# Kernel tuning notes

Hardware: AMD Instinct MI355X
Metric: run time of the kernel (lower is better)

## Reference

```python
import jax, jax.numpy as jnp
import numpy as np

B, C, H, W = 2048, 4, 84, 84
FEAT = 7 * 7 * 64  # 3136, from 84->20->9->7 conv arithmetic
D = 512
E = 6            # num_experts
K = 2            # top_k
A = 12           # output_dim (actions)


def _conv(x, w, b, stride):
    y = jax.lax.conv_general_dilated(
        x, w, window_strides=(stride, stride), padding='VALID',
        dimension_numbers=('NCHW', 'OIHW', 'NCHW'))
    return y + b[None, :, None, None]


def setup_inputs() -> dict:
    key = jax.random.key(0)
    ks = jax.random.split(key, 16)
    s = lambda k, shape, fan: jax.random.normal(k, shape, jnp.float32) * (1.0 / np.sqrt(fan))
    return {
        'x': jax.random.normal(ks[0], (B, C, H, W), jnp.float32),
        'c1_w': s(ks[1], (32, C, 8, 8), C * 64), 'c1_b': jnp.zeros((32,), jnp.float32),
        'c2_w': s(ks[2], (64, 32, 4, 4), 32 * 16), 'c2_b': jnp.zeros((64,), jnp.float32),
        'c3_w': s(ks[3], (64, 64, 3, 3), 64 * 9), 'c3_b': jnp.zeros((64,), jnp.float32),
        'fc_w': s(ks[4], (FEAT, D), FEAT), 'fc_b': jnp.zeros((D,), jnp.float32),
        'gate_w': s(ks[5], (D, E), D), 'gate_b': jnp.zeros((E,), jnp.float32),
        'e_w1': s(ks[6], (E, D, D), D), 'e_b1': jnp.zeros((E, D), jnp.float32),
        'e_w2': s(ks[7], (E, D, D), D), 'e_b2': jnp.zeros((E, D), jnp.float32),
        'e_w3': s(ks[8], (E, D, A), D), 'e_b3': jnp.zeros((E, A), jnp.float32),
    }


def reference(x, c1_w, c1_b, c2_w, c2_b, c3_w, c3_b, fc_w, fc_b,
              gate_w, gate_b, e_w1, e_b1, e_w2, e_b2, e_w3, e_b3):
    # CNN feature extractor (dropout omitted: eval semantics)
    h = jax.nn.relu(_conv(x, c1_w, c1_b, 4))
    h = jax.nn.relu(_conv(h, c2_w, c2_b, 2))
    h = jax.nn.relu(_conv(h, c3_w, c3_b, 1))
    h = h.reshape(h.shape[0], -1)                     # [B, 3136] (C,H,W flatten order)
    f = jax.nn.relu(h @ fc_w + fc_b)                  # [B, 512]

    # Gating: softmax -> top-2 -> renormalize
    gate_probs = jax.nn.softmax(f @ gate_w + gate_b, axis=-1)    # [B, E]
    top_p, top_i = jax.lax.top_k(gate_probs, K)                   # [B, K]
    top_p = top_p / jnp.sum(top_p, axis=-1, keepdims=True)

    # Experts: compute all (tiny MLPs), then gather top-k outputs
    h1 = jax.nn.relu(jnp.einsum('bd,edh->beh', f, e_w1) + e_b1)   # [B, E, D]
    h2 = jax.nn.relu(jnp.einsum('beh,ehg->beg', h1, e_w2) + e_b2) # [B, E, D]
    eo = jnp.einsum('beg,ego->beo', h2, e_w3) + e_b3              # [B, E, A]
    sel = jnp.take_along_axis(eo, top_i[:, :, None], axis=1)      # [B, K, A]
    out = jnp.sum(sel * top_p[:, :, None], axis=1)                # [B, A]
    return out
```

## Files before the change

### kernel.cpp

```cpp
#include <hip/hip_runtime.h>
#include <hip/hip_bf16.h>
#include <math.h>

typedef __attribute__((ext_vector_type(8))) short bf16x8;
typedef __attribute__((ext_vector_type(4))) float f32x4;

__device__ __forceinline__ float b2f(unsigned short u) {
    unsigned int v = ((unsigned int)u) << 16;
    return __uint_as_float(v);
}
__device__ __forceinline__ unsigned short f2b(float f) {
    __hip_bfloat16 h = __float2bfloat16(f);
    return *reinterpret_cast<unsigned short*>(&h);
}
__device__ __forceinline__ void split_trunc(float v, short& h, short& l) {
    unsigned int ui = __float_as_uint(v);
    h = (short)(ui >> 16);
    float hf = __uint_as_float(ui & 0xffff0000u);
    l = (short)f2b(v - hf);
}

__global__ __launch_bounds__(256) void prep_w(
    const float* __restrict__ w1, const float* __restrict__ w2, const float* __restrict__ w3,
    const float* __restrict__ ew3,
    unsigned short* __restrict__ wb1h, unsigned short* __restrict__ wb1l,
    unsigned short* __restrict__ w2h, unsigned short* __restrict__ w2l,
    unsigned short* __restrict__ w3h, unsigned short* __restrict__ w3l,
    float* __restrict__ w3t) {
    int tid = blockIdx.x * 256 + threadIdx.x;
    if (tid < 8192) {
        int k = tid >> 8, r = tid & 255;
        int c = r >> 6, ky = (r >> 3) & 7, kx = r & 7;
        float v = w1[tid];
        unsigned short h = f2b(v);
        int d = ((ky * 2 + (k >> 4)) * 16 + (k & 15)) * 32 + c * 8 + kx;
        wb1h[d] = h;
        wb1l[d] = f2b(v - b2f(h));
    } else if (tid < 8192 + 32768) {
        int i = tid - 8192;
        int n = i >> 9, r = i & 511;
        int c = r >> 4, ky = (r >> 2) & 3, kx = r & 3;
        float v = w2[i];
        unsigned short h = f2b(v);
        int d = ((ky * 4 + kx) * 64 + n) * 32 + c;
        w2h[d] = h;
        w2l[d] = f2b(v - b2f(h));
    } else if (tid < 8192 + 32768 + 36864) {
        int i = tid - 40960;
        int n = i / 576, r = i - n * 576;
        int c = r / 9, s = r - c * 9;
        int ky = s / 3, kx = s - ky * 3;
        float v = w3[i];
        unsigned short h = f2b(v);
        int d = (((ky * 3 + kx) * 2 + (c >> 5)) * 64 + n) * 32 + (c & 31);
        w3h[d] = h;
        w3l[d] = f2b(v - b2f(h));
    } else if (tid < 77824 + 36864) {
        int i = tid - 77824;
        int e = i / 6144, rem = i - e * 6144;
        int a = rem >> 9, k = rem & 511;
        w3t[i] = ew3[e * 6144 + k * 12 + a];
    }
}

__global__ __launch_bounds__(256) void prep_fcw(
    const float* __restrict__ fw, unsigned short* __restrict__ h, unsigned short* __restrict__ l) {
    __shared__ float tile[64][65];
    int k0 = blockIdx.x * 64;
    int n0 = blockIdx.y * 64;
    int tx = threadIdx.x & 63, ty = threadIdx.x >> 6;
#pragma unroll
    for (int j = 0; j < 16; j++) {
        int kk = ty + j * 4;
        int kp = k0 + kk;
        int p = kp >> 6, c = kp & 63;
        tile[kk][tx] = fw[(c * 49 + p) * 512 + n0 + tx];
    }
    __syncthreads();
#pragma unroll
    for (int j = 0; j < 16; j++) {
        int r = ty + j * 4;
        float v = tile[tx][r];
        unsigned short hh = f2b(v);
        long d = (long)(n0 + r) * 3136 + k0 + tx;
        h[d] = hh;
        l[d] = f2b(v - b2f(hh));
    }
}

__global__ __launch_bounds__(256) void prep_ewT(
    const float* __restrict__ ew1, const float* __restrict__ ew2,
    unsigned short* __restrict__ t1, unsigned short* __restrict__ t2) {
    __shared__ float tile[32][33];
    int z = blockIdx.z;
    int e = z % 6;
    const float* src = (z < 6) ? (ew1 + e * 262144) : (ew2 + e * 262144);
    unsigned short* dst = (z < 6) ? (t1 + e * 262144) : (t2 + e * 262144);
    int d0 = blockIdx.y * 32;
    int h0 = blockIdx.x * 32;
    int tx = threadIdx.x, ty = threadIdx.y;
#pragma unroll
    for (int j = 0; j < 4; j++)
        tile[ty + j * 8][tx] = src[(d0 + ty + j * 8) * 512 + h0 + tx];
    __syncthreads();
#pragma unroll
    for (int j = 0; j < 4; j++)
        dst[(h0 + ty + j * 8) * 512 + (d0 + tx)] = f2b(tile[tx][ty + j * 8]);
}

__global__ __launch_bounds__(256, 4) void conv1_k(
    const float* __restrict__ x, const unsigned short* __restrict__ wbh,
    const unsigned short* __restrict__ wbl, const float* __restrict__ b1,
    unsigned short* __restrict__ yhi, unsigned short* __restrict__ ylo) {
    __shared__ bf16x8 wlds[8][4][64];
    int t = threadIdx.x;
    {
        int tab = t >> 6, ln = t & 63;
        const unsigned short* sb = ((tab < 2) ? wbh : wbl) +
            ((ln & 15) * 32 + (ln >> 4) * 8 + (tab & 1) * 512);
#pragma unroll
        for (int k = 0; k < 8; k++)
            wlds[k][tab][ln] = *(const bf16x8*)(sb + k * 1024);
    }
    int wave = t >> 6, lane = t & 63, l16 = lane & 15, quad = lane >> 4;
    int px0 = blockIdx.x * 128 + wave * 32;
    const float* abase[2];
#pragma unroll
    for (int i = 0; i < 2; i++) {
        int px = px0 + i * 16 + l16;
        int n = px / 400;
        int rem = px - n * 400;
        int oy = rem / 20;
        int ox = rem - oy * 20;
        abase[i] = x + (long)n * 28224 + quad * 7056 + oy * 4 * 84 + ox * 4;
    }
    f32x4 acc[2][2];
#pragma unroll
    for (int i = 0; i < 2; i++)
#pragma unroll
        for (int j = 0; j < 2; j++)
#pragma unroll
            for (int r = 0; r < 4; r++) acc[i][j][r] = 0.f;
    __syncthreads();
    float4 buf[3][4];
#pragma unroll
    for (int r = 0; r < 2; r++) {
        __builtin_amdgcn_sched_barrier(0);
#pragma unroll
        for (int i = 0; i < 2; i++) {
            const float* p = abase[i] + r * 84;
            buf[r][i * 2] = *(const float4*)p;
            buf[r][i * 2 + 1] = *(const float4*)(p + 4);
        }
        __builtin_amdgcn_sched_barrier(0);
    }
#pragma unroll
    for (int ky = 0; ky < 8; ky++) {
        if (ky < 6) {
            __builtin_amdgcn_sched_barrier(0);
#pragma unroll
            for (int i = 0; i < 2; i++) {
                const float* p = abase[i] + (ky + 2) * 84;
                buf[(ky + 2) % 3][i * 2] = *(const float4*)p;
                buf[(ky + 2) % 3][i * 2 + 1] = *(const float4*)(p + 4);
            }
            __builtin_amdgcn_sched_barrier(0);
        }
        bf16x8 bh0 = wlds[ky][0][lane];
        bf16x8 bh1 = wlds[ky][1][lane];
        bf16x8 bl0 = wlds[ky][2][lane];
        bf16x8 bl1 = wlds[ky][3][lane];
        bf16x8 ah[2], al[2];
#pragma unroll
        for (int i = 0; i < 2; i++) {
            const float4& c0 = buf[ky % 3][i * 2];
            const float4& c1 = buf[ky % 3][i * 2 + 1];
            float v[8] = {c0.x, c0.y, c0.z, c0.w, c1.x, c1.y, c1.z, c1.w};
#pragma unroll
            for (int j = 0; j < 8; j++) {
                short hh, ll;
                split_trunc(v[j], hh, ll);
                ah[i][j] = hh;
                al[i][j] = ll;
            }
        }
#pragma unroll
        for (int i = 0; i < 2; i++) {
            acc[i][0] = __builtin_amdgcn_mfma_f32_16x16x32_bf16(ah[i], bh0, acc[i][0], 0, 0, 0);
            acc[i][0] = __builtin_amdgcn_mfma_f32_16x16x32_bf16(al[i], bh0, acc[i][0], 0, 0, 0);
            acc[i][0] = __builtin_amdgcn_mfma_f32_16x16x32_bf16(ah[i], bl0, acc[i][0], 0, 0, 0);
            acc[i][1] = __builtin_amdgcn_mfma_f32_16x16x32_bf16(ah[i], bh1, acc[i][1], 0, 0, 0);
            acc[i][1] = __builtin_amdgcn_mfma_f32_16x16x32_bf16(al[i], bh1, acc[i][1], 0, 0, 0);
            acc[i][1] = __builtin_amdgcn_mfma_f32_16x16x32_bf16(ah[i], bl1, acc[i][1], 0, 0, 0);
        }
    }
    float bias0 = b1[l16], bias1 = b1[16 + l16];
#pragma unroll
    for (int i = 0; i < 2; i++) {
#pragma unroll
        for (int r = 0; r < 4; r++) {
            long px = px0 + i * 16 + quad * 4 + r;
            long o = px * 32;
            float v0 = fmaxf(acc[i][0][r] + bias0, 0.f);
            float v1 = fmaxf(acc[i][1][r] + bias1, 0.f);
            short h0, l0, h1, l1;
            split_trunc(v0, h0, l0);
            split_trunc(v1, h1, l1);
            yhi[o + l16] = (unsigned short)h0;
            ylo[o + l16] = (unsigned short)l0;
            yhi[o + 16 + l16] = (unsigned short)h1;
            ylo[o + 16 + l16] = (unsigned short)l1;
        }
    }
}

template <int C, int IH, int IW, int OH, int OW, int S, int KH, int KW>
__global__ __launch_bounds__(256, 2) void convm_k(
    const unsigned short* __restrict__ xhi, const unsigned short* __restrict__ xlo,
    const unsigned short* __restrict__ whi, const unsigned short* __restrict__ wlo,
    const float* __restrict__ bias,
    unsigned short* __restrict__ yhi, unsigned short* __restrict__ ylo) {
    constexpr int CH = C / 32;
    constexpr int NCHUNK = KH * KW * CH;
    __shared__ unsigned short Bst[2][2][4][64][8];
    int t = threadIdx.x;
    int wave = t >> 6, lane = t & 63, l16 = lane & 15, quad = lane >> 4;
    int pxbase = blockIdx.x * 256 + wave * 64;
    long xoff[4];
#pragma unroll
    for (int i = 0; i < 4; i++) {
        int px = pxbase + i * 16 + l16;
        int n = px / (OH * OW);
        int rem = px - n * (OH * OW);
        int oy = rem / OW;
        int ox = rem - oy * OW;
        xoff[i] = (((long)n * IH + oy * S) * IW + ox * S) * C + quad * 8;
    }
    f32x4 acc[4][4];
#pragma unroll
    for (int i = 0; i < 4; i++)
#pragma unroll
        for (int j = 0; j < 4; j++)
#pragma unroll
            for (int r = 0; r < 4; r++) acc[i][j][r] = 0.f;
    long wsrc = (long)lane * 32 + wave * 8;
    uint4 sh = *(const uint4*)(whi + wsrc);
    uint4 sl = *(const uint4*)(wlo + wsrc);
    bf16x8 a_h[4], a_l[4];
    {
#pragma unroll
        for (int i = 0; i < 4; i++) {
            a_h[i] = *(const bf16x8*)(xhi + xoff[i]);
            a_l[i] = *(const bf16x8*)(xlo + xoff[i]);
        }
    }
    *(uint4*)&Bst[0][0][wave][lane][0] = sh;
    *(uint4*)&Bst[0][1][wave][lane][0] = sl;
    asm volatile("s_waitcnt lgkmcnt(0)\n\ts_barrier" ::: "memory");
#pragma unroll
    for (int ck = 0; ck < NCHUNK; ck++) {
        const int cur = ck & 1;
        uint4 nsh, nsl;
        bf16x8 na_h[4], na_l[4];
        if (ck + 1 < NCHUNK) {
            long ws = (long)(ck + 1) * 2048 + lane * 32 + wave * 8;
            nsh = *(const uint4*)(whi + ws);
            nsl = *(const uint4*)(wlo + ws);
            int ck1 = ck + 1;
            int kyx = ck1 / CH;
            int ch = ck1 - kyx * CH;
            int ky = kyx / KW, kx = kyx - ky * KW;
            long k1 = ((long)(ky * IW + kx)) * C + ch * 32;
#pragma unroll
            for (int i = 0; i < 4; i++) {
                na_h[i] = *(const bf16x8*)(xhi + xoff[i] + k1);
                na_l[i] = *(const bf16x8*)(xlo + xoff[i] + k1);
            }
        }
        bf16x8 bh[4], bl[4];
#pragma unroll
        for (int j = 0; j < 4; j++) {
            bh[j] = *(const bf16x8*)&Bst[cur][0][quad][j * 16 + l16][0];
            bl[j] = *(const bf16x8*)&Bst[cur][1][quad][j * 16 + l16][0];
        }
#pragma unroll
        for (int i = 0; i < 4; i++)
#pragma unroll
            for (int j = 0; j < 4; j++) {
                acc[i][j] = __builtin_amdgcn_mfma_f32_16x16x32_bf16(a_h[i], bh[j], acc[i][j], 0, 0, 0);
                acc[i][j] = __builtin_amdgcn_mfma_f32_16x16x32_bf16(a_h[i], bl[j], acc[i][j], 0, 0, 0);
                acc[i][j] = __builtin_amdgcn_mfma_f32_16x16x32_bf16(a_l[i], bh[j], acc[i][j], 0, 0, 0);
            }
        if (ck + 1 < NCHUNK) {
            __builtin_amdgcn_sched_barrier(0);
            *(uint4*)&Bst[cur ^ 1][0][wave][lane][0] = nsh;
            *(uint4*)&Bst[cur ^ 1][1][wave][lane][0] = nsl;
            asm volatile("s_waitcnt lgkmcnt(0)\n\ts_barrier" ::: "memory");
#pragma unroll
            for (int i = 0; i < 4; i++) {
                a_h[i] = na_h[i];
                a_l[i] = na_l[i];
            }
        }
    }
#pragma unroll
    for (int i = 0; i < 4; i++)
#pragma unroll
        for (int j = 0; j < 4; j++) {
            int col = j * 16 + l16;
            float bv = bias[col];
#pragma unroll
            for (int r = 0; r < 4; r++) {
                int prow = pxbase + i * 16 + quad * 4 + r;
                float v = fmaxf(acc[i][j][r] + bv, 0.f);
                unsigned short h = f2b(v);
                yhi[(long)prow * 64 + col] = h;
                ylo[(long)prow * 64 + col] = f2b(v - b2f(h));
            }
        }
}

__global__ __launch_bounds__(64, 3) void fc_k(
    const unsigned short* __restrict__ Ahi, const unsigned short* __restrict__ Alo,
    const unsigned short* __restrict__ Bhi, const unsigned short* __restrict__ Blo,
    float* __restrict__ Cp) {
    int lane = threadIdx.x, l16 = lane & 15, quad = lane >> 4;
    int m0 = blockIdx.x * 64, n0 = blockIdx.y * 64;
    int z = blockIdx.z;
    int kBase = z * 448;
    f32x4 acc[4][4];
#pragma unroll
    for (int i = 0; i < 4; i++)
#pragma unroll
        for (int j = 0; j < 4; j++)
#pragma unroll
            for (int r = 0; r < 4; r++) acc[i][j][r] = 0.f;
#pragma unroll 2
    for (int k0 = kBase; k0 < kBase + 448; k0 += 32) {
        bf16x8 ah[4], al[4], bh[4], bl[4];
#pragma unroll
        for (int i = 0; i < 4; i++) {
            long a = (long)(m0 + i * 16 + l16) * 3136 + k0 + quad * 8;
            ah[i] = *(const bf16x8*)(Ahi + a);
            al[i] = *(const bf16x8*)(Alo + a);
        }
#pragma unroll
        for (int j = 0; j < 4; j++) {
            long b = (long)(n0 + j * 16 + l16) * 3136 + k0 + quad * 8;
            bh[j] = *(const bf16x8*)(Bhi + b);
            bl[j] = *(const bf16x8*)(Blo + b);
        }
#pragma unroll
        for (int i = 0; i < 4; i++)
#pragma unroll
            for (int j = 0; j < 4; j++) {
                acc[i][j] = __builtin_amdgcn_mfma_f32_16x16x32_bf16(ah[i], bh[j], acc[i][j], 0, 0, 0);
                acc[i][j] = __builtin_amdgcn_mfma_f32_16x16x32_bf16(ah[i], bl[j], acc[i][j], 0, 0, 0);
                acc[i][j] = __builtin_amdgcn_mfma_f32_16x16x32_bf16(al[i], bh[j], acc[i][j], 0, 0, 0);
            }
    }
    float* Cz = Cp + (long)z * 1048576;
#pragma unroll
    for (int i = 0; i < 4; i++)
#pragma unroll
        for (int j = 0; j < 4; j++) {
            int col = n0 + j * 16 + l16;
#pragma unroll
            for (int r = 0; r < 4; r++) {
                int row = m0 + i * 16 + quad * 4 + r;
                Cz[row * 512 + col] = acc[i][j][r];
            }
        }
}

__global__ __launch_bounds__(256) void fc_fin(
    const float* __restrict__ Cp, const float* __restrict__ bias,
    float* __restrict__ f, unsigned short* __restrict__ fb, int* __restrict__ cnt) {
    if (blockIdx.x == 0 && threadIdx.x < 8) cnt[threadIdx.x] = 0;
    int tid = blockIdx.x * 256 + threadIdx.x;
    int col = tid & 511;
    float v = bias[col];
#pragma unroll
    for (int z = 0; z < 7; z++) v += Cp[tid + (long)z * 1048576];
    v = fmaxf(v, 0.f);
    f[tid] = v;
    fb[tid] = f2b(v);
}

__global__ __launch_bounds__(256) void gate_k(
    const float* __restrict__ f, const float* __restrict__ gw, const float* __restrict__ gb,
    int* __restrict__ topi, float* __restrict__ topp,
    int* __restrict__ cnt, int* __restrict__ rowlist, int* __restrict__ slotp) {
    int wave = threadIdx.x >> 6, lane = threadIdx.x & 63;
    int row = blockIdx.x * 4 + wave;
    float fv[8];
#pragma unroll
    for (int j = 0; j < 8; j++) fv[j] = f[row * 512 + lane + 64 * j];
    float lg[6];
#pragma unroll
    for (int e = 0; e < 6; e++) {
        float a = 0.f;
#pragma unroll
        for (int j = 0; j < 8; j++) a += fv[j] * gw[(lane + 64 * j) * 6 + e];
#pragma unroll
        for (int off = 32; off > 0; off >>= 1) a += __shfl_xor(a, off, 64);
        lg[e] = a + gb[e];
    }
    if (lane == 0) {
        int i1 = 0;
        float v1 = lg[0];
#pragma unroll
        for (int e = 1; e < 6; e++)
            if (lg[e] > v1) { v1 = lg[e]; i1 = e; }
        int i2 = (i1 == 0) ? 1 : 0;
        float v2 = lg[i2];
#pragma unroll
        for (int e = 0; e < 6; e++)
            if (e != i1 && lg[e] > v2) { v2 = lg[e]; i2 = e; }
        float pa = 1.f / (1.f + expf(v2 - v1));
        topi[row * 2] = i1;
        topi[row * 2 + 1] = i2;
        topp[row * 2] = pa;
        topp[row * 2 + 1] = 1.f - pa;
        int s1 = atomicAdd(cnt + i1, 1);
        int s2 = atomicAdd(cnt + i2, 1);
        rowlist[i1 * 2048 + s1] = row;
        rowlist[i2 * 2048 + s2] = row;
        slotp[row * 2] = s1;
        slotp[row * 2 + 1] = s2;
    }
}

__global__ __launch_bounds__(64, 4) void moe_gemm(
    const unsigned short* __restrict__ A, long aStride,
    const unsigned short* __restrict__ Bt, const float* __restrict__ bias,
    unsigned short* __restrict__ C,
    const int* __restrict__ cnt, const int* __restrict__ rowlist) {
    int e = blockIdx.z;
    int ne = cnt[e];
    int m0 = blockIdx.x * 64;
    if (m0 >= ne) return;
    const unsigned short* Ae = A + (long)e * aStride;
    const unsigned short* Be = Bt + (long)e * 262144;
    const float* be = bias + e * 512;
    unsigned short* Ce = C + (long)e * 2048 * 512;
    int lane = threadIdx.x, l16 = lane & 15, quad = lane >> 4;
    int n0 = blockIdx.y * 64;
    int arow[4];
#pragma unroll
    for (int i = 0; i < 4; i++) {
        int slot = m0 + i * 16 + l16;
        arow[i] = rowlist ? ((slot < ne) ? rowlist[e * 2048 + slot] : 0) : slot;
    }
    f32x4 acc[4][4];
#pragma unroll
    for (int i = 0; i < 4; i++)
#pragma unroll
        for (int j = 0; j < 4; j++)
#pragma unroll
            for (int r = 0; r < 4; r++) acc[i][j][r] = 0.f;
#pragma unroll 4
    for (int k0 = 0; k0 < 512; k0 += 32) {
        bf16x8 a[4], b[4];
#pragma unroll
        for (int i = 0; i < 4; i++)
            a[i] = *(const bf16x8*)(Ae + (long)arow[i] * 512 + k0 + quad * 8);
#pragma unroll
        for (int j = 0; j < 4; j++)
            b[j] = *(const bf16x8*)(Be + (long)(n0 + j * 16 + l16) * 512 + k0 + quad * 8);
#pragma unroll
        for (int i = 0; i < 4; i++)
#pragma unroll
            for (int j = 0; j < 4; j++)
                acc[i][j] = __builtin_amdgcn_mfma_f32_16x16x32_bf16(a[i], b[j], acc[i][j], 0, 0, 0);
    }
#pragma unroll
    for (int i = 0; i < 4; i++)
#pragma unroll
        for (int j = 0; j < 4; j++) {
            int col = n0 + j * 16 + l16;
            float bcol = be[col];
#pragma unroll
            for (int r = 0; r < 4; r++) {
                int row = m0 + i * 16 + quad * 4 + r;
                float v = fmaxf(acc[i][j][r] + bcol, 0.f);
                Ce[(long)row * 512 + col] = f2b(v);
            }
        }
}

__global__ __launch_bounds__(256) void combine_k(
    const unsigned short* __restrict__ h2, const float* __restrict__ w3t,
    const float* __restrict__ b3, const int* __restrict__ topi,
    const float* __restrict__ topp, const int* __restrict__ slotp,
    float* __restrict__ out) {
    int b = blockIdx.x * 4 + (threadIdx.x >> 6);
    int lane = threadIdx.x & 63;
    int e0 = topi[b * 2], e1 = topi[b * 2 + 1];
    float p0 = topp[b * 2], p1 = topp[b * 2 + 1];
    int s0 = slotp[b * 2], s1 = slotp[b * 2 + 1];
    float r[12];
#pragma unroll
    for (int a = 0; a < 12; a++) r[a] = 0.f;
#pragma unroll
    for (int j = 0; j < 2; j++) {
        int e = j ? e1 : e0;
        int s = j ? s1 : s0;
        float p = j ? p1 : p0;
        const unsigned short* hp = h2 + ((long)e * 2048 + s) * 512 + lane * 8;
        bf16x8 hv = *(const bf16x8*)hp;
        float hf[8];
#pragma unroll
        for (int q = 0; q < 8; q++) hf[q] = b2f((unsigned short)hv[q]);
        const float* wb = w3t + e * 6144 + lane * 8;
#pragma unroll
        for (int a = 0; a < 12; a++) {
            float4 w0 = *(const float4*)(wb + a * 512);
            float4 w1 = *(const float4*)(wb + a * 512 + 4);
            float acc = hf[0] * w0.x + hf[1] * w0.y + hf[2] * w0.z + hf[3] * w0.w +
                        hf[4] * w1.x + hf[5] * w1.y + hf[6] * w1.z + hf[7] * w1.w;
            r[a] += p * acc;
        }
    }
#pragma unroll
    for (int a = 0; a < 12; a++)
#pragma unroll
        for (int off = 32; off > 0; off >>= 1) r[a] += __shfl_xor(r[a], off, 64);
    float v = 0.f;
#pragma unroll
    for (int a = 0; a < 12; a++)
        if (lane == a) v = r[a];
    if (lane < 12)
        out[b * 12 + lane] = v + p0 * b3[e0 * 12 + lane] + p1 * b3[e1 * 12 + lane];
}

extern "C" void kernel_launch(void* const* d_in, const int* in_sizes, int n_in,
                              void* d_out, int out_size, void* d_ws, size_t ws_size,
                              hipStream_t stream) {
    const float* x   = (const float*)d_in[0];
    const float* c1w = (const float*)d_in[1];
    const float* c1b = (const float*)d_in[2];
    const float* c2w = (const float*)d_in[3];
    const float* c2b = (const float*)d_in[4];
    const float* c3w = (const float*)d_in[5];
    const float* c3b = (const float*)d_in[6];
    const float* fcw = (const float*)d_in[7];
    const float* fcb = (const float*)d_in[8];
    const float* gw  = (const float*)d_in[9];
    const float* gb  = (const float*)d_in[10];
    const float* ew1 = (const float*)d_in[11];
    const float* eb1 = (const float*)d_in[12];
    const float* ew2 = (const float*)d_in[13];
    const float* eb2 = (const float*)d_in[14];
    const float* ew3 = (const float*)d_in[15];
    const float* eb3 = (const float*)d_in[16];

    char* ws = (char*)d_ws;
    unsigned short* y1hi = (unsigned short*)(ws + 0L);
    unsigned short* y1lo = (unsigned short*)(ws + 52428800L);
    unsigned short* f3hi = (unsigned short*)(ws + 0L);
    unsigned short* f3lo = (unsigned short*)(ws + 12845056L);
    int*   cnt           = (int*)(ws + 26214400L);
    int*   rowlist       = (int*)(ws + 26214464L);
    int*   slotp         = (int*)(ws + 26263616L);
    unsigned short* y2hi = (unsigned short*)(ws + 104857600L);
    unsigned short* y2lo = (unsigned short*)(ws + 126091264L);
    unsigned short* h1   = (unsigned short*)(ws + 104857600L);
    unsigned short* h2   = (unsigned short*)(ws + 117440512L);
    float* f             = (float*)(ws + 147324928L);
    unsigned short* fb   = (unsigned short*)(ws + 151519232L);
    int*   topi          = (int*)(ws + 153616384L);
    float* topp          = (float*)(ws + 153632768L);
    unsigned short* w2h  = (unsigned short*)(ws + 153681920L);
    unsigned short* w2l  = (unsigned short*)(ws + 153747456L);
    unsigned short* w3h  = (unsigned short*)(ws + 153812992L);
    unsigned short* w3l  = (unsigned short*)(ws + 153886720L);
    unsigned short* fcwh = (unsigned short*)(ws + 153960448L);
    unsigned short* fcwl = (unsigned short*)(ws + 157171712L);
    unsigned short* ew1t = (unsigned short*)(ws + 160382976L);
    unsigned short* ew2t = (unsigned short*)(ws + 163528704L);
    float* w3t           = (float*)(ws + 166674432L);
    float* Cp            = (float*)(ws + 166821888L);
    unsigned short* wb1h = (unsigned short*)(ws + 196182016L);
    unsigned short* wb1l = (unsigned short*)(ws + 196198400L);
    float* out = (float*)d_out;

    hipLaunchKernelGGL(prep_w, dim3(448), dim3(256), 0, stream, c1w, c2w, c3w, ew3,
                       wb1h, wb1l, w2h, w2l, w3h, w3l, w3t);
    hipLaunchKernelGGL(prep_fcw, dim3(49, 8), dim3(256), 0, stream, fcw, fcwh, fcwl);
    hipLaunchKernelGGL(prep_ewT, dim3(16, 16, 12), dim3(32, 8), 0, stream, ew1, ew2, ew1t, ew2t);
    hipLaunchKernelGGL(conv1_k, dim3(6400), dim3(256), 0, stream, x, wb1h, wb1l, c1b, y1hi, y1lo);
    hipLaunchKernelGGL((convm_k<32, 20, 20, 9, 9, 2, 4, 4>), dim3(648), dim3(256), 0, stream,
                       y1hi, y1lo, w2h, w2l, c2b, y2hi, y2lo);
    hipLaunchKernelGGL((convm_k<64, 9, 9, 7, 7, 1, 3, 3>), dim3(392), dim3(256), 0, stream,
                       y2hi, y2lo, w3h, w3l, c3b, f3hi, f3lo);
    hipLaunchKernelGGL(fc_k, dim3(32, 8, 7), dim3(64), 0, stream, f3hi, f3lo, fcwh, fcwl, Cp);
    hipLaunchKernelGGL(fc_fin, dim3(4096), dim3(256), 0, stream, Cp, fcb, f, fb, cnt);
    hipLaunchKernelGGL(gate_k, dim3(512), dim3(256), 0, stream, f, gw, gb, topi, topp,
                       cnt, rowlist, slotp);
    hipLaunchKernelGGL(moe_gemm, dim3(32, 8, 6), dim3(64), 0, stream, fb, 0L, ew1t, eb1, h1,
                       cnt, rowlist);
    hipLaunchKernelGGL(moe_gemm, dim3(32, 8, 6), dim3(64), 0, stream, h1, 1048576L, ew2t, eb2, h2,
                       cnt, (const int*)nullptr);
    hipLaunchKernelGGL(combine_k, dim3(512), dim3(256), 0, stream, h2, w3t, eb3, topi, topp,
                       slotp, out);
}
```

Before: 693.8 us.

## Merge prep kernels, fuse fc finalize with gating, deepen conv1 prefetch, swizzle blocks

```diff
diff --git a/kernel.cpp b/kernel.cpp
--- a/kernel.cpp
+++ b/kernel.cpp
@@ -20,92 +20,93 @@
     l = (short)f2b(v - hf);
 }
 
-__global__ __launch_bounds__(256) void prep_w(
+__global__ __launch_bounds__(256) void prep_all(
     const float* __restrict__ w1, const float* __restrict__ w2, const float* __restrict__ w3,
-    const float* __restrict__ ew3,
+    const float* __restrict__ ew3, const float* __restrict__ fw,
+    const float* __restrict__ ew1, const float* __restrict__ ew2,
     unsigned short* __restrict__ wb1h, unsigned short* __restrict__ wb1l,
     unsigned short* __restrict__ w2h, unsigned short* __restrict__ w2l,
     unsigned short* __restrict__ w3h, unsigned short* __restrict__ w3l,
-    float* __restrict__ w3t) {
-    int tid = blockIdx.x * 256 + threadIdx.x;
-    if (tid < 8192) {
-        int k = tid >> 8, r = tid & 255;
-        int c = r >> 6, ky = (r >> 3) & 7, kx = r & 7;
-        float v = w1[tid];
-        unsigned short h = f2b(v);
-        int d = ((ky * 2 + (k >> 4)) * 16 + (k & 15)) * 32 + c * 8 + kx;
-        wb1h[d] = h;
-        wb1l[d] = f2b(v - b2f(h));
-    } else if (tid < 8192 + 32768) {
-        int i = tid - 8192;
-        int n = i >> 9, r = i & 511;
-        int c = r >> 4, ky = (r >> 2) & 3, kx = r & 3;
-        float v = w2[i];
-        unsigned short h = f2b(v);
-        int d = ((ky * 4 + kx) * 64 + n) * 32 + c;
-        w2h[d] = h;
-        w2l[d] = f2b(v - b2f(h));
-    } else if (tid < 8192 + 32768 + 36864) {
-        int i = tid - 40960;
-        int n = i / 576, r = i - n * 576;
-        int c = r / 9, s = r - c * 9;
-        int ky = s / 3, kx = s - ky * 3;
-        float v = w3[i];
-        unsigned short h = f2b(v);
-        int d = (((ky * 3 + kx) * 2 + (c >> 5)) * 64 + n) * 32 + (c & 31);
-        w3h[d] = h;
-        w3l[d] = f2b(v - b2f(h));
-    } else if (tid < 77824 + 36864) {
-        int i = tid - 77824;
-        int e = i / 6144, rem = i - e * 6144;
-        int a = rem >> 9, k = rem & 511;
-        w3t[i] = ew3[e * 6144 + k * 12 + a];
-    }
-}
-
-__global__ __launch_bounds__(256) void prep_fcw(
-    const float* __restrict__ fw, unsigned short* __restrict__ h, unsigned short* __restrict__ l) {
-    __shared__ float tile[64][65];
-    int k0 = blockIdx.x * 64;
-    int n0 = blockIdx.y * 64;
-    int tx = threadIdx.x & 63, ty = threadIdx.x >> 6;
-#pragma unroll
-    for (int j = 0; j < 16; j++) {
-        int kk = ty + j * 4;
-        int kp = k0 + kk;
-        int p = kp >> 6, c = kp & 63;
-        tile[kk][tx] = fw[(c * 49 + p) * 512 + n0 + tx];
-    }
-    __syncthreads();
-#pragma unroll
-    for (int j = 0; j < 16; j++) {
-        int r = ty + j * 4;
-        float v = tile[tx][r];
-        unsigned short hh = f2b(v);
-        long d = (long)(n0 + r) * 3136 + k0 + tx;
-        h[d] = hh;
-        l[d] = f2b(v - b2f(hh));
-    }
-}
-
-__global__ __launch_bounds__(256) void prep_ewT(
-    const float* __restrict__ ew1, const float* __restrict__ ew2,
+    float* __restrict__ w3t,
+    unsigned short* __restrict__ fh, unsigned short* __restrict__ fl,
     unsigned short* __restrict__ t1, unsigned short* __restrict__ t2) {
-    __shared__ float tile[32][33];
-    int z = blockIdx.z;
-    int e = z % 6;
-    const float* src = (z < 6) ? (ew1 + e * 262144) : (ew2 + e * 262144);
-    unsigned short* dst = (z < 6) ? (t1 + e * 262144) : (t2 + e * 262144);
-    int d0 = blockIdx.y * 32;
-    int h0 = blockIdx.x * 32;
-    int tx = threadIdx.x, ty = threadIdx.y;
-#pragma unroll
-    for (int j = 0; j < 4; j++)
-        tile[ty + j * 8][tx] = src[(d0 + ty + j * 8) * 512 + h0 + tx];
-    __syncthreads();
-#pragma unroll
-    for (int j = 0; j < 4; j++)
-        dst[(h0 + ty + j * 8) * 512 + (d0 + tx)] = f2b(tile[tx][ty + j * 8]);
+    __shared__ float lds_f[64 * 65];
+    int b = blockIdx.x;
+    int t = threadIdx.x;
+    if (b < 448) {
+        int tid = b * 256 + t;
+        if (tid < 8192) {
+            int k = tid >> 8, r = tid & 255;
+            int c = r >> 6, ky = (r >> 3) & 7, kx = r & 7;
+            float v = w1[tid];
+            unsigned short h = f2b(v);
+            int d = ((ky * 2 + (k >> 4)) * 16 + (k & 15)) * 32 + c * 8 + kx;
+            wb1h[d] = h;
+            wb1l[d] = f2b(v - b2f(h));
+        } else if (tid < 8192 + 32768) {
+            int i = tid - 8192;
+            int n = i >> 9, r = i & 511;
+            int c = r >> 4, ky = (r >> 2) & 3, kx = r & 3;
+            float v = w2[i];
+            unsigned short h = f2b(v);
+            int d = ((ky * 4 + kx) * 64 + n) * 32 + c;
+            w2h[d] = h;
+            w2l[d] = f2b(v - b2f(h));
+        } else if (tid < 8192 + 32768 + 36864) {
+            int i = tid - 40960;
+            int n = i / 576, r = i - n * 576;
+            int c = r / 9, s = r - c * 9;
+            int ky = s / 3, kx = s - ky * 3;
+            float v = w3[i];
+            unsigned short h = f2b(v);
+            int d = (((ky * 3 + kx) * 2 + (c >> 5)) * 64 + n) * 32 + (c & 31);
+            w3h[d] = h;
+            w3l[d] = f2b(v - b2f(h));
+        } else if (tid < 77824 + 36864) {
+            int i = tid - 77824;
+            int e = i / 6144, rem = i - e * 6144;
+            int a = rem >> 9, k = rem & 511;
+            w3t[i] = ew3[e * 6144 + k * 12 + a];
+        }
+    } else if (b < 840) {
+        int bx = b - 448;
+        int k0 = (bx % 49) * 64;
+        int n0 = (bx / 49) * 64;
+        int tx = t & 63, ty = t >> 6;
+#pragma unroll
+        for (int j = 0; j < 16; j++) {
+            int kk = ty + j * 4;
+            int kp = k0 + kk;
+            int p = kp >> 6, c = kp & 63;
+            lds_f[kk * 65 + tx] = fw[(c * 49 + p) * 512 + n0 + tx];
+        }
+        __syncthreads();
+#pragma unroll
+        for (int j = 0; j < 16; j++) {
+            int r = ty + j * 4;
+            float v = lds_f[tx * 65 + r];
+            unsigned short hh = f2b(v);
+            long d = (long)(n0 + r) * 3136 + k0 + tx;
+            fh[d] = hh;
+            fl[d] = f2b(v - b2f(hh));
+        }
+    } else {
+        int i = b - 840;
+        int h0 = (i & 15) * 32;
+        int d0 = ((i >> 4) & 15) * 32;
+        int z = i >> 8;
+        int e = z % 6;
+        const float* src = (z < 6) ? (ew1 + e * 262144) : (ew2 + e * 262144);
+        unsigned short* dst = (z < 6) ? (t1 + e * 262144) : (t2 + e * 262144);
+        int tx = t & 31, ty = t >> 5;
+#pragma unroll
+        for (int j = 0; j < 4; j++)
+            lds_f[(ty + j * 8) * 33 + tx] = src[(d0 + ty + j * 8) * 512 + h0 + tx];
+        __syncthreads();
+#pragma unroll
+        for (int j = 0; j < 4; j++)
+            dst[(h0 + ty + j * 8) * 512 + (d0 + tx)] = f2b(lds_f[tx * 33 + ty + j * 8]);
+    }
 }
 
 __global__ __launch_bounds__(256, 4) void conv1_k(
@@ -122,8 +123,9 @@
         for (int k = 0; k < 8; k++)
             wlds[k][tab][ln] = *(const bf16x8*)(sb + k * 1024);
     }
+    int swz = (blockIdx.x & 7) * 800 + (blockIdx.x >> 3);
     int wave = t >> 6, lane = t & 63, l16 = lane & 15, quad = lane >> 4;
-    int px0 = blockIdx.x * 128 + wave * 32;
+    int px0 = swz * 128 + wave * 32;
     const float* abase[2];
 #pragma unroll
     for (int i = 0; i < 2; i++) {
@@ -142,9 +144,9 @@
 #pragma unroll
             for (int r = 0; r < 4; r++) acc[i][j][r] = 0.f;
     __syncthreads();
-    float4 buf[3][4];
-#pragma unroll
-    for (int r = 0; r < 2; r++) {
+    float4 buf[4][4];
+#pragma unroll
+    for (int r = 0; r < 3; r++) {
         __builtin_amdgcn_sched_barrier(0);
 #pragma unroll
         for (int i = 0; i < 2; i++) {
@@ -156,13 +158,13 @@
     }
 #pragma unroll
     for (int ky = 0; ky < 8; ky++) {
-        if (ky < 6) {
+        if (ky < 5) {
             __builtin_amdgcn_sched_barrier(0);
 #pragma unroll
             for (int i = 0; i < 2; i++) {
-                const float* p = abase[i] + (ky + 2) * 84;
-                buf[(ky + 2) % 3][i * 2] = *(const float4*)p;
-                buf[(ky + 2) % 3][i * 2 + 1] = *(const float4*)(p + 4);
+                const float* p = abase[i] + (ky + 3) * 84;
+                buf[(ky + 3) & 3][i * 2] = *(const float4*)p;
+                buf[(ky + 3) & 3][i * 2 + 1] = *(const float4*)(p + 4);
             }
             __builtin_amdgcn_sched_barrier(0);
         }
@@ -173,8 +175,8 @@
         bf16x8 ah[2], al[2];
 #pragma unroll
         for (int i = 0; i < 2; i++) {
-            const float4& c0 = buf[ky % 3][i * 2];
-            const float4& c1 = buf[ky % 3][i * 2 + 1];
+            const float4& c0 = buf[ky & 3][i * 2];
+            const float4& c1 = buf[ky & 3][i * 2 + 1];
             float v[8] = {c0.x, c0.y, c0.z, c0.w, c1.x, c1.y, c1.z, c1.w};
 #pragma unroll
             for (int j = 0; j < 8; j++) {
@@ -323,7 +325,9 @@
 __global__ __launch_bounds__(64, 3) void fc_k(
     const unsigned short* __restrict__ Ahi, const unsigned short* __restrict__ Alo,
     const unsigned short* __restrict__ Bhi, const unsigned short* __restrict__ Blo,
-    float* __restrict__ Cp) {
+    float* __restrict__ Cp, int* __restrict__ cnt) {
+    if (blockIdx.x == 0 && blockIdx.y == 0 && blockIdx.z == 0 && threadIdx.x < 8)
+        cnt[threadIdx.x] = 0;
     int lane = threadIdx.x, l16 = lane & 15, quad = lane >> 4;
     int m0 = blockIdx.x * 64, n0 = blockIdx.y * 64;
     int z = blockIdx.z;
@@ -373,61 +377,64 @@
         }
 }
 
-__global__ __launch_bounds__(256) void fc_fin(
+__global__ __launch_bounds__(256) void fin_gate(
     const float* __restrict__ Cp, const float* __restrict__ bias,
-    float* __restrict__ f, unsigned short* __restrict__ fb, int* __restrict__ cnt) {
-    if (blockIdx.x == 0 && threadIdx.x < 8) cnt[threadIdx.x] = 0;
-    int tid = blockIdx.x * 256 + threadIdx.x;
-    int col = tid & 511;
-    float v = bias[col];
-#pragma unroll
-    for (int z = 0; z < 7; z++) v += Cp[tid + (long)z * 1048576];
-    v = fmaxf(v, 0.f);
-    f[tid] = v;
-    fb[tid] = f2b(v);
-}
-
-__global__ __launch_bounds__(256) void gate_k(
-    const float* __restrict__ f, const float* __restrict__ gw, const float* __restrict__ gb,
-    int* __restrict__ topi, float* __restrict__ topp,
+    const float* __restrict__ gw, const float* __restrict__ gb,
+    unsigned short* __restrict__ fb, int* __restrict__ topi, float* __restrict__ topp,
     int* __restrict__ cnt, int* __restrict__ rowlist, int* __restrict__ slotp) {
-    int wave = threadIdx.x >> 6, lane = threadIdx.x & 63;
-    int row = blockIdx.x * 4 + wave;
-    float fv[8];
-#pragma unroll
-    for (int j = 0; j < 8; j++) fv[j] = f[row * 512 + lane + 64 * j];
-    float lg[6];
-#pragma unroll
-    for (int e = 0; e < 6; e++) {
-        float a = 0.f;
-#pragma unroll
-        for (int j = 0; j < 8; j++) a += fv[j] * gw[(lane + 64 * j) * 6 + e];
-#pragma unroll
-        for (int off = 32; off > 0; off >>= 1) a += __shfl_xor(a, off, 64);
-        lg[e] = a + gb[e];
-    }
-    if (lane == 0) {
-        int i1 = 0;
-        float v1 = lg[0];
-#pragma unroll
-        for (int e = 1; e < 6; e++)
-            if (lg[e] > v1) { v1 = lg[e]; i1 = e; }
-        int i2 = (i1 == 0) ? 1 : 0;
-        float v2 = lg[i2];
-#pragma unroll
-        for (int e = 0; e < 6; e++)
-            if (e != i1 && lg[e] > v2) { v2 = lg[e]; i2 = e; }
-        float pa = 1.f / (1.f + expf(v2 - v1));
-        topi[row * 2] = i1;
-        topi[row * 2 + 1] = i2;
-        topp[row * 2] = pa;
-        topp[row * 2 + 1] = 1.f - pa;
-        int s1 = atomicAdd(cnt + i1, 1);
-        int s2 = atomicAdd(cnt + i2, 1);
-        rowlist[i1 * 2048 + s1] = row;
-        rowlist[i2 * 2048 + s2] = row;
-        slotp[row * 2] = s1;
-        slotp[row * 2 + 1] = s2;
+    __shared__ float frow[512];
+    int row = blockIdx.x;
+    int t = threadIdx.x;
+#pragma unroll
+    for (int s = 0; s < 2; s++) {
+        int c = t + s * 256;
+        long base = (long)row * 512 + c;
+        float v = bias[c];
+#pragma unroll
+        for (int z = 0; z < 7; z++) v += Cp[base + (long)z * 1048576];
+        v = fmaxf(v, 0.f);
+        fb[base] = f2b(v);
+        frow[c] = v;
+    }
+    __syncthreads();
+    if (t < 64) {
+        int lane = t;
+        float fv[8];
+#pragma unroll
+        for (int j = 0; j < 8; j++) fv[j] = frow[lane + 64 * j];
+        float lg[6];
+#pragma unroll
+        for (int e = 0; e < 6; e++) {
+            float a = 0.f;
+#pragma unroll
+            for (int j = 0; j < 8; j++) a += fv[j] * gw[(lane + 64 * j) * 6 + e];
+#pragma unroll
+            for (int off = 32; off > 0; off >>= 1) a += __shfl_xor(a, off, 64);
+            lg[e] = a + gb[e];
+        }
+        if (lane == 0) {
+            int i1 = 0;
+            float v1 = lg[0];
+#pragma unroll
+            for (int e = 1; e < 6; e++)
+                if (lg[e] > v1) { v1 = lg[e]; i1 = e; }
+            int i2 = (i1 == 0) ? 1 : 0;
+            float v2 = lg[i2];
+#pragma unroll
+            for (int e = 0; e < 6; e++)
+                if (e != i1 && lg[e] > v2) { v2 = lg[e]; i2 = e; }
+            float pa = 1.f / (1.f + expf(v2 - v1));
+            topi[row * 2] = i1;
+            topi[row * 2 + 1] = i2;
+            topp[row * 2] = pa;
+            topp[row * 2 + 1] = 1.f - pa;
+            int s1 = atomicAdd(cnt + i1, 1);
+            int s2 = atomicAdd(cnt + i2, 1);
+            rowlist[i1 * 2048 + s1] = row;
+            rowlist[i2 * 2048 + s2] = row;
+            slotp[row * 2] = s1;
+            slotp[row * 2 + 1] = s2;
+        }
     }
 }
 
@@ -567,7 +574,6 @@
     unsigned short* y2lo = (unsigned short*)(ws + 126091264L);
     unsigned short* h1   = (unsigned short*)(ws + 104857600L);
     unsigned short* h2   = (unsigned short*)(ws + 117440512L);
-    float* f             = (float*)(ws + 147324928L);
     unsigned short* fb   = (unsigned short*)(ws + 151519232L);
     int*   topi          = (int*)(ws + 153616384L);
     float* topp          = (float*)(ws + 153632768L);
@@ -585,19 +591,17 @@
     unsigned short* wb1l = (unsigned short*)(ws + 196198400L);
     float* out = (float*)d_out;
 
-    hipLaunchKernelGGL(prep_w, dim3(448), dim3(256), 0, stream, c1w, c2w, c3w, ew3,
-                       wb1h, wb1l, w2h, w2l, w3h, w3l, w3t);
-    hipLaunchKernelGGL(prep_fcw, dim3(49, 8), dim3(256), 0, stream, fcw, fcwh, fcwl);
-    hipLaunchKernelGGL(prep_ewT, dim3(16, 16, 12), dim3(32, 8), 0, stream, ew1, ew2, ew1t, ew2t);
+    hipLaunchKernelGGL(prep_all, dim3(3912), dim3(256), 0, stream,
+                       c1w, c2w, c3w, ew3, fcw, ew1, ew2,
+                       wb1h, wb1l, w2h, w2l, w3h, w3l, w3t, fcwh, fcwl, ew1t, ew2t);
     hipLaunchKernelGGL(conv1_k, dim3(6400), dim3(256), 0, stream, x, wb1h, wb1l, c1b, y1hi, y1lo);
     hipLaunchKernelGGL((convm_k<32, 20, 20, 9, 9, 2, 4, 4>), dim3(648), dim3(256), 0, stream,
                        y1hi, y1lo, w2h, w2l, c2b, y2hi, y2lo);
     hipLaunchKernelGGL((convm_k<64, 9, 9, 7, 7, 1, 3, 3>), dim3(392), dim3(256), 0, stream,
                        y2hi, y2lo, w3h, w3l, c3b, f3hi, f3lo);
-    hipLaunchKernelGGL(fc_k, dim3(32, 8, 7), dim3(64), 0, stream, f3hi, f3lo, fcwh, fcwl, Cp);
-    hipLaunchKernelGGL(fc_fin, dim3(4096), dim3(256), 0, stream, Cp, fcb, f, fb, cnt);
-    hipLaunchKernelGGL(gate_k, dim3(512), dim3(256), 0, stream, f, gw, gb, topi, topp,
-                       cnt, rowlist, slotp);
+    hipLaunchKernelGGL(fc_k, dim3(32, 8, 7), dim3(64), 0, stream, f3hi, f3lo, fcwh, fcwl, Cp, cnt);
+    hipLaunchKernelGGL(fin_gate, dim3(2048), dim3(256), 0, stream, Cp, fcb, gw, gb,
+                       fb, topi, topp, cnt, rowlist, slotp);
     hipLaunchKernelGGL(moe_gemm, dim3(32, 8, 6), dim3(64), 0, stream, fb, 0L, ew1t, eb1, h1,
                        cnt, rowlist);
     hipLaunchKernelGGL(moe_gemm, dim3(32, 8, 6), dim3(64), 0, stream, h1, 1048576L, ew2t, eb2, h2,
```

Result: no change. 685.9 us (-1.1%).
